# Performance work log

Measured on AMD Instinct MI355X. Metric: run time of the kernel, lower is better.

## Reference

```python
import jax, jax.numpy as jnp
import numpy as np

N = 50000
E = 1600000
F_IN = 2304
H1, D1 = 8, 8   # layer-1 heads, per-head dim (concat -> 64)
C = 5           # num classes, layer-2 heads=1


def setup_inputs() -> dict:
    key = jax.random.key(0)
    ks = jax.random.split(key, 10)
    s1 = 1.0 / np.sqrt(F_IN)
    s2 = 1.0 / np.sqrt(H1 * D1)
    return {
        "x": jax.random.normal(ks[0], (N, F_IN), dtype=jnp.float32),
        "edge_index": jax.random.randint(ks[1], (2, E), 0, N, dtype=jnp.int32),
        "W1": jax.random.normal(ks[2], (F_IN, H1 * D1), dtype=jnp.float32) * s1,
        "att_src1": jax.random.normal(ks[3], (H1, D1), dtype=jnp.float32) * s2,
        "att_dst1": jax.random.normal(ks[4], (H1, D1), dtype=jnp.float32) * s2,
        "b1": jnp.zeros((H1 * D1,), dtype=jnp.float32),
        "W2": jax.random.normal(ks[5], (H1 * D1, C), dtype=jnp.float32) * s2,
        "att_src2": jax.random.normal(ks[6], (1, C), dtype=jnp.float32) * 0.4,
        "att_dst2": jax.random.normal(ks[7], (1, C), dtype=jnp.float32) * 0.4,
        "b2": jnp.zeros((C,), dtype=jnp.float32),
    }


def _gat_layer(x, src, dst, W, att_src, att_dst, bias, heads, d, n):
    # Projection: [n, heads, d]
    h = (x @ W).reshape(n, heads, d)
    # Per-node attention terms, gathered per edge: [Etot, heads]
    a_src = jnp.einsum("nhd,hd->nh", h, att_src)
    a_dst = jnp.einsum("nhd,hd->nh", h, att_dst)
    logit = jax.nn.leaky_relu(a_src[src] + a_dst[dst], negative_slope=0.2)
    # Softmax over incoming edges of each dst node (segment softmax)
    m = jax.ops.segment_max(logit, dst, num_segments=n)
    p = jnp.exp(logit - m[dst])
    z = jax.ops.segment_sum(p, dst, num_segments=n)
    alpha = p / (z[dst] + 1e-16)
    # Weighted message scatter-add: [n, heads, d]
    out = jax.ops.segment_sum(h[src] * alpha[:, :, None], dst, num_segments=n)
    return out.reshape(n, heads * d) + bias


def reference(x, edge_index, W1, att_src1, att_dst1, b1, W2, att_src2, att_dst2, b2):
    n = x.shape[0]
    # PyG GATConv default: add self-loops
    loops = jnp.arange(n, dtype=edge_index.dtype)
    src = jnp.concatenate([edge_index[0], loops])
    dst = jnp.concatenate([edge_index[1], loops])
    h1 = _gat_layer(x, src, dst, W1, att_src1, att_dst1, b1, H1, D1, n)
    h2 = _gat_layer(h1, src, dst, W2, att_src2, att_dst2, b2, 1, C, n)
    return jax.nn.log_softmax(h2, axis=1)
```

## Files before the change

### kernel.cpp

```cpp
#include <hip/hip_runtime.h>

#define N_NODES 50000
#define N_EDGES 1600000
#define ETOT (N_EDGES + N_NODES)
#define F_IN 2304
#define HD 64
#define H1 8
#define D1 8
#define NC 5
#define NB_SCAN ((N_NODES + 255) / 256)
#define KB (F_IN / 32)
#define NTILE (N_NODES / 16)

typedef __attribute__((ext_vector_type(8))) short short8v;
typedef __attribute__((ext_vector_type(4))) float f32x4;

__device__ __forceinline__ float lrelu(float x) { return x > 0.f ? x : 0.2f * x; }

__device__ __forceinline__ unsigned short f2bf(float f) {
    unsigned u = __float_as_uint(f);
    u += 0x7fffu + ((u >> 16) & 1u);
    return (unsigned short)(u >> 16);
}
__device__ __forceinline__ float bf2f(unsigned short u) {
    return __uint_as_float(((unsigned)u) << 16);
}

__device__ __forceinline__ void edge_sd(const int* __restrict__ ei, int e, int& s, int& t) {
    if (e < N_EDGES) { s = ei[e]; t = ei[N_EDGES + e]; }
    else { s = e - N_EDGES; t = s; }
}

__global__ void hist_kernel(const int* __restrict__ ei, unsigned* __restrict__ deg,
                            int* __restrict__ epos) {
    int e = blockIdx.x * blockDim.x + threadIdx.x;
    if (e >= ETOT) return;
    int s, t; edge_sd(ei, e, s, t);
    epos[e] = (int)atomicAdd(&deg[t], 1u);
}

__global__ void scan_block_kernel(const unsigned* __restrict__ deg,
                                  unsigned* __restrict__ rowptr,
                                  unsigned* __restrict__ bsum) {
    __shared__ unsigned sm[256];
    int i = blockIdx.x * 256 + threadIdx.x;
    unsigned v = (i < N_NODES) ? deg[i] : 0u;
    sm[threadIdx.x] = v;
    __syncthreads();
    #pragma unroll
    for (int off = 1; off < 256; off <<= 1) {
        unsigned u = (threadIdx.x >= off) ? sm[threadIdx.x - off] : 0u;
        __syncthreads();
        sm[threadIdx.x] += u;
        __syncthreads();
    }
    if (i < N_NODES) rowptr[i] = sm[threadIdx.x] - v;
    if (threadIdx.x == 255) bsum[blockIdx.x] = sm[255];
}

__global__ void scan_top_kernel(unsigned* __restrict__ bsum, unsigned* __restrict__ boff) {
    __shared__ unsigned sm[256];
    int i = threadIdx.x;
    unsigned v = (i < NB_SCAN) ? bsum[i] : 0u;
    sm[i] = v;
    __syncthreads();
    #pragma unroll
    for (int off = 1; off < 256; off <<= 1) {
        unsigned u = (i >= off) ? sm[i - off] : 0u;
        __syncthreads();
        sm[i] += u;
        __syncthreads();
    }
    if (i < NB_SCAN) boff[i] = sm[i] - v;
}

__global__ void scan_add_kernel(unsigned* __restrict__ rowptr, const unsigned* __restrict__ boff) {
    int i = blockIdx.x * 256 + threadIdx.x;
    if (i < N_NODES) rowptr[i] += boff[blockIdx.x];
    if (i == 0) rowptr[N_NODES] = ETOT;
}

__global__ void fill_kernel(const int* __restrict__ ei, const unsigned* __restrict__ rowptr,
                            const int* __restrict__ epos, int* __restrict__ col) {
    int e = blockIdx.x * blockDim.x + threadIdx.x;
    if (e >= ETOT) return;
    int s, t; edge_sd(ei, e, s, t);
    col[rowptr[t] + epos[e]] = s;
}

__global__ void packW_kernel(const float* __restrict__ W, short* __restrict__ Wp) {
    int idx = blockIdx.x * 256 + threadIdx.x;
    if (idx >= KB * 4 * 64) return;
    int lane = idx & 63;
    int cb = (idx >> 6) & 3;
    int k0 = idx >> 8;
    int colg = cb * 16 + (lane & 15);
    int kbase = k0 * 32 + (lane >> 4) * 8;
    short8v v;
    #pragma unroll
    for (int j = 0; j < 8; j++)
        v[j] = (short)f2bf(W[(kbase + j) * HD + colg]);
    *reinterpret_cast<short8v*>(&Wp[(long)idx * 8]) = v;
}

__global__ __launch_bounds__(256) void gemm1_mfma(const float* __restrict__ x,
                                                  const short* __restrict__ Wp,
                                                  const float* __restrict__ asrc_w,
                                                  const float* __restrict__ adst_w,
                                                  unsigned short* __restrict__ hb,
                                                  float* __restrict__ a_src,
                                                  float* __restrict__ a_dst) {
    int wave = threadIdx.x >> 6;
    int lane = threadIdx.x & 63;
    int tile = blockIdx.x * 4 + wave;
    if (tile >= NTILE) return;
    int arow = tile * 16 + (lane & 15);
    const f32x4* xp = reinterpret_cast<const f32x4*>(x + (long)arow * F_IN + (lane >> 4) * 8);
    const short8v* wp = reinterpret_cast<const short8v*>(Wp) + lane;
    f32x4 acc0 = {}, acc1 = {}, acc2 = {}, acc3 = {};
    f32x4 x0 = __builtin_nontemporal_load(xp);
    f32x4 x1 = __builtin_nontemporal_load(xp + 1);
    f32x4 y0 = __builtin_nontemporal_load(xp + 8);
    f32x4 y1 = __builtin_nontemporal_load(xp + 9);
    xp += 16;
    for (int k0 = 0; k0 < KB - 2; k0++) {
        short8v b0 = wp[0 * 64];
        short8v b1 = wp[1 * 64];
        short8v b2 = wp[2 * 64];
        short8v b3 = wp[3 * 64];
        wp += 4 * 64;
        f32x4 z0 = __builtin_nontemporal_load(xp);
        f32x4 z1 = __builtin_nontemporal_load(xp + 1);
        xp += 8;
        short8v af;
        #pragma unroll
        for (int j = 0; j < 4; j++) af[j] = (short)f2bf(x0[j]);
        #pragma unroll
        for (int j = 0; j < 4; j++) af[4 + j] = (short)f2bf(x1[j]);
        acc0 = __builtin_amdgcn_mfma_f32_16x16x32_bf16(af, b0, acc0, 0, 0, 0);
        acc1 = __builtin_amdgcn_mfma_f32_16x16x32_bf16(af, b1, acc1, 0, 0, 0);
        acc2 = __builtin_amdgcn_mfma_f32_16x16x32_bf16(af, b2, acc2, 0, 0, 0);
        acc3 = __builtin_amdgcn_mfma_f32_16x16x32_bf16(af, b3, acc3, 0, 0, 0);
        x0 = y0; x1 = y1; y0 = z0; y1 = z1;
    }
    #pragma unroll
    for (int tb = 0; tb < 2; tb++) {
        short8v b0 = wp[0 * 64];
        short8v b1 = wp[1 * 64];
        short8v b2 = wp[2 * 64];
        short8v b3 = wp[3 * 64];
        wp += 4 * 64;
        short8v af;
        #pragma unroll
        for (int j = 0; j < 4; j++) af[j] = (short)f2bf(tb == 0 ? x0[j] : y0[j]);
        #pragma unroll
        for (int j = 0; j < 4; j++) af[4 + j] = (short)f2bf(tb == 0 ? x1[j] : y1[j]);
        acc0 = __builtin_amdgcn_mfma_f32_16x16x32_bf16(af, b0, acc0, 0, 0, 0);
        acc1 = __builtin_amdgcn_mfma_f32_16x16x32_bf16(af, b1, acc1, 0, 0, 0);
        acc2 = __builtin_amdgcn_mfma_f32_16x16x32_bf16(af, b2, acc2, 0, 0, 0);
        acc3 = __builtin_amdgcn_mfma_f32_16x16x32_bf16(af, b3, acc3, 0, 0, 0);
    }
    int c0 = lane & 15;
    long rbase = (long)(tile * 16 + (lane >> 4) * 4) * HD;
    #pragma unroll
    for (int r = 0; r < 4; r++) {
        hb[rbase + r * HD + c0]      = f2bf(acc0[r]);
        hb[rbase + r * HD + 16 + c0] = f2bf(acc1[r]);
        hb[rbase + r * HD + 32 + c0] = f2bf(acc2[r]);
        hb[rbase + r * HD + 48 + c0] = f2bf(acc3[r]);
    }
    float wsv[4], wdv[4];
    #pragma unroll
    for (int cb = 0; cb < 4; cb++) {
        wsv[cb] = asrc_w[cb * 16 + c0];
        wdv[cb] = adst_w[cb * 16 + c0];
    }
    int nbase = tile * 16 + (lane >> 4) * 4;
    #pragma unroll
    for (int r = 0; r < 4; r++) {
        float a[4] = {acc0[r], acc1[r], acc2[r], acc3[r]};
        #pragma unroll
        for (int cb = 0; cb < 4; cb++) {
            float vs = a[cb] * wsv[cb];
            float vd = a[cb] * wdv[cb];
            vs += __shfl_xor(vs, 1, 64); vd += __shfl_xor(vd, 1, 64);
            vs += __shfl_xor(vs, 2, 64); vd += __shfl_xor(vd, 2, 64);
            vs += __shfl_xor(vs, 4, 64); vd += __shfl_xor(vd, 4, 64);
            if ((c0 & 7) == 0) {
                int hh = 2 * cb + (c0 >> 3);
                a_src[(nbase + r) * 8 + hh] = vs;
                a_dst[(nbase + r) * 8 + hh] = vd;
            }
        }
    }
}

__global__ __launch_bounds__(256) void agg1_proj2_kernel(const unsigned* __restrict__ rowptr,
                                                         const int* __restrict__ col,
                                                         const float* __restrict__ a_src,
                                                         const float* __restrict__ a_dst,
                                                         const unsigned short* __restrict__ hb,
                                                         const float* __restrict__ b1,
                                                         const float* __restrict__ W2,
                                                         const float* __restrict__ asrc2_w,
                                                         const float* __restrict__ adst2_w,
                                                         float* __restrict__ h2p,
                                                         float* __restrict__ a_src2,
                                                         float* __restrict__ a_dst2) {
    int n = blockIdx.x * 4 + (threadIdx.x >> 6);
    if (n >= N_NODES) return;
    int k = threadIdx.x & 63;
    int hh = k >> 3;
    float ad = a_dst[n * 8 + hh];
    int r0 = rowptr[n], r1 = rowptr[n + 1];
    float acc = 0.f, z = 0.f;
    int e = r0;
    for (; e + 3 < r1; e += 4) {
        int s0 = col[e], s1 = col[e + 1], s2 = col[e + 2], s3 = col[e + 3];
        float as0 = a_src[s0 * 8 + hh];
        float as1 = a_src[s1 * 8 + hh];
        float as2 = a_src[s2 * 8 + hh];
        float as3 = a_src[s3 * 8 + hh];
        unsigned short u0 = hb[(long)s0 * 64 + k];
        unsigned short u1 = hb[(long)s1 * 64 + k];
        unsigned short u2 = hb[(long)s2 * 64 + k];
        unsigned short u3 = hb[(long)s3 * 64 + k];
        float p0 = __expf(lrelu(as0 + ad));
        float p1 = __expf(lrelu(as1 + ad));
        float p2 = __expf(lrelu(as2 + ad));
        float p3 = __expf(lrelu(as3 + ad));
        z += (p0 + p1) + (p2 + p3);
        acc += p0 * bf2f(u0) + p1 * bf2f(u1) + p2 * bf2f(u2) + p3 * bf2f(u3);
    }
    for (; e < r1; ++e) {
        int s0 = col[e];
        float p0 = __expf(lrelu(a_src[s0 * 8 + hh] + ad));
        z += p0;
        acc += p0 * bf2f(hb[(long)s0 * 64 + k]);
    }
    float v = acc / (z + 1e-16f) + b1[k];
    float part[NC];
    #pragma unroll
    for (int c = 0; c < NC; c++) part[c] = v * W2[k * NC + c];
    #pragma unroll
    for (int off = 32; off >= 1; off >>= 1)
        #pragma unroll
        for (int c = 0; c < NC; c++) part[c] += __shfl_xor(part[c], off, 64);
    if (k == 0) {
        float as = 0.f, ad2 = 0.f;
        f32x4 h0; float h4;
        #pragma unroll
        for (int c = 0; c < NC; c++) {
            as  += part[c] * asrc2_w[c];
            ad2 += part[c] * adst2_w[c];
        }
        h0[0] = part[0]; h0[1] = part[1]; h0[2] = part[2]; h0[3] = part[3];
        h4 = part[4];
        *reinterpret_cast<f32x4*>(&h2p[n * 8]) = h0;
        h2p[n * 8 + 4] = h4;
        h2p[n * 8 + 5] = 0.f; h2p[n * 8 + 6] = 0.f; h2p[n * 8 + 7] = 0.f;
        a_src2[n] = as;
        a_dst2[n] = ad2;
    }
}

__global__ void agg2_kernel(const unsigned* __restrict__ rowptr, const int* __restrict__ col,
                            const float* __restrict__ a_src2, const float* __restrict__ a_dst2,
                            const float* __restrict__ h2p, const float* __restrict__ b2,
                            float* __restrict__ y) {
    int n = blockIdx.x * blockDim.x + threadIdx.x;
    if (n >= N_NODES) return;
    float ad = a_dst2[n];
    int r0 = rowptr[n], r1 = rowptr[n + 1];
    float acc[NC] = {};
    float z = 0.f;
    for (int e = r0; e < r1; ++e) {
        int s = col[e];
        float p = __expf(lrelu(a_src2[s] + ad));
        z += p;
        const f32x4* hp = reinterpret_cast<const f32x4*>(&h2p[s * 8]);
        f32x4 v0 = hp[0];
        float v4 = h2p[s * 8 + 4];
        acc[0] += p * v0[0]; acc[1] += p * v0[1]; acc[2] += p * v0[2];
        acc[3] += p * v0[3]; acc[4] += p * v4;
    }
    float inv = 1.f / (z + 1e-16f);
    float l[NC], mx = -3.4e38f;
    #pragma unroll
    for (int c = 0; c < NC; c++) {
        l[c] = acc[c] * inv + b2[c];
        mx = fmaxf(mx, l[c]);
    }
    float ssum = 0.f;
    #pragma unroll
    for (int c = 0; c < NC; c++) ssum += __expf(l[c] - mx);
    float lse = __logf(ssum);
    #pragma unroll
    for (int c = 0; c < NC; c++) y[n * NC + c] = l[c] - mx - lse;
}

extern "C" void kernel_launch(void* const* d_in, const int* in_sizes, int n_in,
                              void* d_out, int out_size, void* d_ws, size_t ws_size,
                              hipStream_t stream) {
    const float* x        = (const float*)d_in[0];
    const int*   ei       = (const int*)d_in[1];
    const float* W1       = (const float*)d_in[2];
    const float* att_src1 = (const float*)d_in[3];
    const float* att_dst1 = (const float*)d_in[4];
    const float* b1       = (const float*)d_in[5];
    const float* W2       = (const float*)d_in[6];
    const float* att_src2 = (const float*)d_in[7];
    const float* att_dst2 = (const float*)d_in[8];
    const float* b2       = (const float*)d_in[9];
    float* y = (float*)d_out;

    unsigned short* hb = (unsigned short*)d_ws;
    float* a_src1  = (float*)(hb + (long)N_NODES * 64);
    float* a_dst1  = a_src1 + N_NODES * 8;
    float* h2p     = a_dst1 + N_NODES * 8;
    float* a_src2  = h2p + (long)N_NODES * 8;
    float* a_dst2  = a_src2 + N_NODES;
    unsigned* deg    = (unsigned*)(a_dst2 + N_NODES);
    unsigned* rowptr = deg + N_NODES;
    unsigned* bsum   = rowptr + N_NODES + 1;
    unsigned* boff   = bsum + 256;
    int*      col    = (int*)(boff + 256);
    int*      epos   = col + ETOT;
    short*    Wp     = (short*)(epos + ETOT);

    hipMemsetAsync(deg, 0, N_NODES * sizeof(unsigned), stream);
    hist_kernel<<<(ETOT + 255) / 256, 256, 0, stream>>>(ei, deg, epos);
    packW_kernel<<<(KB * 4 * 64 + 255) / 256, 256, 0, stream>>>(W1, Wp);
    scan_block_kernel<<<NB_SCAN, 256, 0, stream>>>(deg, rowptr, bsum);
    scan_top_kernel<<<1, 256, 0, stream>>>(bsum, boff);
    scan_add_kernel<<<NB_SCAN, 256, 0, stream>>>(rowptr, boff);
    fill_kernel<<<(ETOT + 255) / 256, 256, 0, stream>>>(ei, rowptr, epos, col);

    gemm1_mfma<<<(NTILE + 3) / 4, 256, 0, stream>>>(x, Wp, att_src1, att_dst1, hb, a_src1, a_dst1);
    agg1_proj2_kernel<<<(N_NODES + 3) / 4, 256, 0, stream>>>(rowptr, col, a_src1, a_dst1, hb,
                                                             b1, W2, att_src2, att_dst2,
                                                             h2p, a_src2, a_dst2);

    agg2_kernel<<<(N_NODES + 255) / 256, 256, 0, stream>>>(rowptr, col, a_src2, a_dst2, h2p, b2, y);
}
```

Baseline: 382.1 us.

## Overlap degree histogram with GEMM in one fused launch, merge scan kernels

Folds the edge-degree histogram into extra blocks of the layer-1 GEMM launch. The atomic-heavy histogram can then run alongside the memory-bound x streaming instead of as a separate serial kernel. It also merges the scan-top and scan-add kernels into one, with each block redoing the small top-level scan. The layer-2 aggregation loop is unrolled by four to issue more independent gathers. Risks are contention between histogram blocks and GEMM blocks for bandwidth, and the GEMM waves being placed later in dispatch.

Measured after the change: 337.8 us, median of 2. 1.13x faster.

```diff
diff --git a/kernel.cpp b/kernel.cpp
--- a/kernel.cpp
+++ b/kernel.cpp
@@ -11,6 +11,8 @@
 #define NB_SCAN ((N_NODES + 255) / 256)
 #define KB (F_IN / 32)
 #define NTILE (N_NODES / 16)
+#define GEMM_BLOCKS ((NTILE + 3) / 4)
+#define HIST_BLOCKS 2048
 
 typedef __attribute__((ext_vector_type(8))) short short8v;
 typedef __attribute__((ext_vector_type(4))) float f32x4;
@@ -29,63 +31,6 @@
 __device__ __forceinline__ void edge_sd(const int* __restrict__ ei, int e, int& s, int& t) {
     if (e < N_EDGES) { s = ei[e]; t = ei[N_EDGES + e]; }
     else { s = e - N_EDGES; t = s; }
-}
-
-__global__ void hist_kernel(const int* __restrict__ ei, unsigned* __restrict__ deg,
-                            int* __restrict__ epos) {
-    int e = blockIdx.x * blockDim.x + threadIdx.x;
-    if (e >= ETOT) return;
-    int s, t; edge_sd(ei, e, s, t);
-    epos[e] = (int)atomicAdd(&deg[t], 1u);
-}
-
-__global__ void scan_block_kernel(const unsigned* __restrict__ deg,
-                                  unsigned* __restrict__ rowptr,
-                                  unsigned* __restrict__ bsum) {
-    __shared__ unsigned sm[256];
-    int i = blockIdx.x * 256 + threadIdx.x;
-    unsigned v = (i < N_NODES) ? deg[i] : 0u;
-    sm[threadIdx.x] = v;
-    __syncthreads();
-    #pragma unroll
-    for (int off = 1; off < 256; off <<= 1) {
-        unsigned u = (threadIdx.x >= off) ? sm[threadIdx.x - off] : 0u;
-        __syncthreads();
-        sm[threadIdx.x] += u;
-        __syncthreads();
-    }
-    if (i < N_NODES) rowptr[i] = sm[threadIdx.x] - v;
-    if (threadIdx.x == 255) bsum[blockIdx.x] = sm[255];
-}
-
-__global__ void scan_top_kernel(unsigned* __restrict__ bsum, unsigned* __restrict__ boff) {
-    __shared__ unsigned sm[256];
-    int i = threadIdx.x;
-    unsigned v = (i < NB_SCAN) ? bsum[i] : 0u;
-    sm[i] = v;
-    __syncthreads();
-    #pragma unroll
-    for (int off = 1; off < 256; off <<= 1) {
-        unsigned u = (i >= off) ? sm[i - off] : 0u;
-        __syncthreads();
-        sm[i] += u;
-        __syncthreads();
-    }
-    if (i < NB_SCAN) boff[i] = sm[i] - v;
-}
-
-__global__ void scan_add_kernel(unsigned* __restrict__ rowptr, const unsigned* __restrict__ boff) {
-    int i = blockIdx.x * 256 + threadIdx.x;
-    if (i < N_NODES) rowptr[i] += boff[blockIdx.x];
-    if (i == 0) rowptr[N_NODES] = ETOT;
-}
-
-__global__ void fill_kernel(const int* __restrict__ ei, const unsigned* __restrict__ rowptr,
-                            const int* __restrict__ epos, int* __restrict__ col) {
-    int e = blockIdx.x * blockDim.x + threadIdx.x;
-    if (e >= ETOT) return;
-    int s, t; edge_sd(ei, e, s, t);
-    col[rowptr[t] + epos[e]] = s;
 }
 
 __global__ void packW_kernel(const float* __restrict__ W, short* __restrict__ Wp) {
@@ -103,13 +48,24 @@
     *reinterpret_cast<short8v*>(&Wp[(long)idx * 8]) = v;
 }
 
-__global__ __launch_bounds__(256) void gemm1_mfma(const float* __restrict__ x,
-                                                  const short* __restrict__ Wp,
-                                                  const float* __restrict__ asrc_w,
-                                                  const float* __restrict__ adst_w,
-                                                  unsigned short* __restrict__ hb,
-                                                  float* __restrict__ a_src,
-                                                  float* __restrict__ a_dst) {
+__global__ __launch_bounds__(256) void fat_gemm_hist(const float* __restrict__ x,
+                                                     const short* __restrict__ Wp,
+                                                     const float* __restrict__ asrc_w,
+                                                     const float* __restrict__ adst_w,
+                                                     unsigned short* __restrict__ hb,
+                                                     float* __restrict__ a_src,
+                                                     float* __restrict__ a_dst,
+                                                     const int* __restrict__ ei,
+                                                     unsigned* __restrict__ deg,
+                                                     int* __restrict__ epos) {
+    if (blockIdx.x >= GEMM_BLOCKS) {
+        int b = blockIdx.x - GEMM_BLOCKS;
+        for (long e = (long)b * 256 + threadIdx.x; e < ETOT; e += (long)HIST_BLOCKS * 256) {
+            int s, t; edge_sd(ei, (int)e, s, t);
+            epos[e] = (int)atomicAdd(&deg[t], 1u);
+        }
+        return;
+    }
     int wave = threadIdx.x >> 6;
     int lane = threadIdx.x & 63;
     int tile = blockIdx.x * 4 + wave;
@@ -193,6 +149,53 @@
             }
         }
     }
+}
+
+__global__ void scan_block_kernel(const unsigned* __restrict__ deg,
+                                  unsigned* __restrict__ rowptr,
+                                  unsigned* __restrict__ bsum) {
+    __shared__ unsigned sm[256];
+    int i = blockIdx.x * 256 + threadIdx.x;
+    unsigned v = (i < N_NODES) ? deg[i] : 0u;
+    sm[threadIdx.x] = v;
+    __syncthreads();
+    #pragma unroll
+    for (int off = 1; off < 256; off <<= 1) {
+        unsigned u = (threadIdx.x >= off) ? sm[threadIdx.x - off] : 0u;
+        __syncthreads();
+        sm[threadIdx.x] += u;
+        __syncthreads();
+    }
+    if (i < N_NODES) rowptr[i] = sm[threadIdx.x] - v;
+    if (threadIdx.x == 255) bsum[blockIdx.x] = sm[255];
+}
+
+__global__ void scan_addtop_kernel(unsigned* __restrict__ rowptr,
+                                   const unsigned* __restrict__ bsum) {
+    __shared__ unsigned sm[256];
+    int tid = threadIdx.x;
+    unsigned v = (tid < NB_SCAN) ? bsum[tid] : 0u;
+    sm[tid] = v;
+    __syncthreads();
+    #pragma unroll
+    for (int off = 1; off < 256; off <<= 1) {
+        unsigned u = (tid >= off) ? sm[tid - off] : 0u;
+        __syncthreads();
+        sm[tid] += u;
+        __syncthreads();
+    }
+    unsigned prefix = (blockIdx.x == 0) ? 0u : sm[blockIdx.x - 1];
+    int i = blockIdx.x * 256 + tid;
+    if (i < N_NODES) rowptr[i] += prefix;
+    if (i == 0) rowptr[N_NODES] = ETOT;
+}
+
+__global__ void fill_kernel(const int* __restrict__ ei, const unsigned* __restrict__ rowptr,
+                            const int* __restrict__ epos, int* __restrict__ col) {
+    int e = blockIdx.x * blockDim.x + threadIdx.x;
+    if (e >= ETOT) return;
+    int s, t; edge_sd(ei, e, s, t);
+    col[rowptr[t] + epos[e]] = s;
 }
 
 __global__ __launch_bounds__(256) void agg1_proj2_kernel(const unsigned* __restrict__ rowptr,
@@ -248,16 +251,15 @@
         for (int c = 0; c < NC; c++) part[c] += __shfl_xor(part[c], off, 64);
     if (k == 0) {
         float as = 0.f, ad2 = 0.f;
-        f32x4 h0; float h4;
         #pragma unroll
         for (int c = 0; c < NC; c++) {
             as  += part[c] * asrc2_w[c];
             ad2 += part[c] * adst2_w[c];
         }
+        f32x4 h0;
         h0[0] = part[0]; h0[1] = part[1]; h0[2] = part[2]; h0[3] = part[3];
-        h4 = part[4];
         *reinterpret_cast<f32x4*>(&h2p[n * 8]) = h0;
-        h2p[n * 8 + 4] = h4;
+        h2p[n * 8 + 4] = part[4];
         h2p[n * 8 + 5] = 0.f; h2p[n * 8 + 6] = 0.f; h2p[n * 8 + 7] = 0.f;
         a_src2[n] = as;
         a_dst2[n] = ad2;
@@ -274,12 +276,30 @@
     int r0 = rowptr[n], r1 = rowptr[n + 1];
     float acc[NC] = {};
     float z = 0.f;
-    for (int e = r0; e < r1; ++e) {
+    int e = r0;
+    for (; e + 3 < r1; e += 4) {
+        int s0 = col[e], s1 = col[e + 1], s2 = col[e + 2], s3 = col[e + 3];
+        float as0 = a_src2[s0], as1 = a_src2[s1], as2 = a_src2[s2], as3 = a_src2[s3];
+        f32x4 v0 = *reinterpret_cast<const f32x4*>(&h2p[s0 * 8]);
+        f32x4 v1 = *reinterpret_cast<const f32x4*>(&h2p[s1 * 8]);
+        f32x4 v2 = *reinterpret_cast<const f32x4*>(&h2p[s2 * 8]);
+        f32x4 v3 = *reinterpret_cast<const f32x4*>(&h2p[s3 * 8]);
+        float w0 = h2p[s0 * 8 + 4], w1 = h2p[s1 * 8 + 4], w2 = h2p[s2 * 8 + 4], w3 = h2p[s3 * 8 + 4];
+        float p0 = __expf(lrelu(as0 + ad));
+        float p1 = __expf(lrelu(as1 + ad));
+        float p2 = __expf(lrelu(as2 + ad));
+        float p3 = __expf(lrelu(as3 + ad));
+        z += (p0 + p1) + (p2 + p3);
+        #pragma unroll
+        for (int c = 0; c < 4; c++)
+            acc[c] += p0 * v0[c] + p1 * v1[c] + p2 * v2[c] + p3 * v3[c];
+        acc[4] += p0 * w0 + p1 * w1 + p2 * w2 + p3 * w3;
+    }
+    for (; e < r1; ++e) {
         int s = col[e];
         float p = __expf(lrelu(a_src2[s] + ad));
         z += p;
-        const f32x4* hp = reinterpret_cast<const f32x4*>(&h2p[s * 8]);
-        f32x4 v0 = hp[0];
+        f32x4 v0 = *reinterpret_cast<const f32x4*>(&h2p[s * 8]);
         float v4 = h2p[s * 8 + 4];
         acc[0] += p * v0[0]; acc[1] += p * v0[1]; acc[2] += p * v0[2];
         acc[3] += p * v0[3]; acc[4] += p * v4;
@@ -323,23 +343,22 @@
     unsigned* deg    = (unsigned*)(a_dst2 + N_NODES);
     unsigned* rowptr = deg + N_NODES;
     unsigned* bsum   = rowptr + N_NODES + 1;
-    unsigned* boff   = bsum + 256;
-    int*      col    = (int*)(boff + 256);
+    int*      col    = (int*)(bsum + 256);
     int*      epos   = col + ETOT;
     short*    Wp     = (short*)(epos + ETOT);
 
     hipMemsetAsync(deg, 0, N_NODES * sizeof(unsigned), stream);
-    hist_kernel<<<(ETOT + 255) / 256, 256, 0, stream>>>(ei, deg, epos);
     packW_kernel<<<(KB * 4 * 64 + 255) / 256, 256, 0, stream>>>(W1, Wp);
+
+    fat_gemm_hist<<<GEMM_BLOCKS + HIST_BLOCKS, 256, 0, stream>>>(
+        x, Wp, att_src1, att_dst1, hb, a_src1, a_dst1, ei, deg, epos);
+
     scan_block_kernel<<<NB_SCAN, 256, 0, stream>>>(deg, rowptr, bsum);
-    scan_top_kernel<<<1, 256, 0, stream>>>(bsum, boff);
-    scan_add_kernel<<<NB_SCAN, 256, 0, stream>>>(rowptr, boff);
+    scan_addtop_kernel<<<NB_SCAN, 256, 0, stream>>>(rowptr, bsum);
     fill_kernel<<<(ETOT + 255) / 256, 256, 0, stream>>>(ei, rowptr, epos, col);
 
-    gemm1_mfma<<<(NTILE + 3) / 4, 256, 0, stream>>>(x, Wp, att_src1, att_dst1, hb, a_src1, a_dst1);
     agg1_proj2_kernel<<<(N_NODES + 3) / 4, 256, 0, stream>>>(rowptr, col, a_src1, a_dst1, hb,
                                                              b1, W2, att_src2, att_dst2,
                                                              h2p, a_src2, a_dst2);
-
     agg2_kernel<<<(N_NODES + 255) / 256, 256, 0, stream>>>(rowptr, col, a_src2, a_dst2, h2p, b2, y);
 }
```
